# Kernel optimization log

Hardware: AMD Instinct MI355X
Metric: run time of the kernel (lower is better)

## Reference

```python
import jax, jax.numpy as jnp
import numpy as np

B, T_OBS, H, L, D = 4096, 8, 512, 2, 2


def _gates(x, h, c, Wih, Whh, b):
    # PyTorch LSTM gate order: i, f, g, o
    g = x @ Wih.T + h @ Whh.T + b
    i, f, gg, o = jnp.split(g, 4, axis=-1)
    c_new = jax.nn.sigmoid(f) * c + jax.nn.sigmoid(i) * jnp.tanh(gg)
    h_new = jax.nn.sigmoid(o) * jnp.tanh(c_new)
    return h_new, c_new


def _run_lstm(x, Wih, Whh, b):
    # stacked batch_first LSTM, zero initial state; x: [B,T,H]
    n_layers = Wih.shape[0]
    hs, cs = [], []
    for l in range(n_layers):
        def step(carry, xt, l=l):
            h, c = carry
            h, c = _gates(xt, h, c, Wih[l], Whh[l], b[l])
            return (h, c), h
        init = (jnp.zeros((x.shape[0], Whh.shape[-1]), x.dtype),
                jnp.zeros((x.shape[0], Whh.shape[-1]), x.dtype))
        (h, c), ys = jax.lax.scan(step, init, jnp.swapaxes(x, 0, 1))
        x = jnp.swapaxes(ys, 0, 1)
        hs.append(h)
        cs.append(c)
    return x, jnp.stack(hs), jnp.stack(cs)


def setup_inputs() -> dict:
    key = jax.random.key(0)
    ks = jax.random.split(key, 12)
    s = 1.0 / np.sqrt(H)
    inp = {
        "obs": jax.random.normal(ks[0], (B, T_OBS, D), jnp.float32),
        "obsVel": jax.random.normal(ks[1], (B, T_OBS, D), jnp.float32),
        "mean": jax.random.normal(ks[2], (D,), jnp.float32),
        "std": jnp.ones((D,), jnp.float32),
        "pred_len": 12,
        "enc_W": jax.random.normal(ks[3], (D, H), jnp.float32) * s,
        "enc_b": jnp.zeros((H,), jnp.float32),
        "dec_W": jax.random.normal(ks[4], (H, D), jnp.float32) * s,
        "dec_b": jnp.zeros((D,), jnp.float32),
        "lstm_Wih": jax.random.normal(ks[5], (L, 4 * H, H), jnp.float32) * s,
        "lstm_Whh": jax.random.normal(ks[6], (L, 4 * H, H), jnp.float32) * s,
        "lstm_b": jnp.zeros((L, 4 * H), jnp.float32),
        "cell_Wih": jax.random.normal(ks[7], (L, 4 * H, H), jnp.float32) * s,
        "cell_Whh": jax.random.normal(ks[8], (L, 4 * H, H), jnp.float32) * s,
        "cell_b": jnp.zeros((L, 4 * H), jnp.float32),
    }
    return inp


def reference(obs, obsVel, mean, std, pred_len, enc_W, enc_b, dec_W, dec_b,
              lstm_Wih, lstm_Whh, lstm_b, cell_Wih, cell_Whh, cell_b):
    inp = (obsVel - mean) / std                      # [B,T,2]
    embed = inp @ enc_W + enc_b                      # [B,T,H]
    output, hs, cs = _run_lstm(embed, lstm_Wih, lstm_Whh, lstm_b)
    inner = output[:, -1, :]                         # [B,H]

    def decode_step(carry, _):
        hs, cs, inner = carry
        def layer(inner, xs):
            Wih, Whh, b, h, c = xs
            h2, c2 = _gates(inner, h, c, Wih, Whh, b)
            return h2, (h2, c2)
        inner2, (hs2, cs2) = jax.lax.scan(
            layer, inner, (cell_Wih, cell_Whh, cell_b, hs, cs))
        return (hs2, cs2, inner2), inner2

    _, steps = jax.lax.scan(decode_step, (hs, cs, inner), None,
                            length=pred_len - 1)     # [P-1,B,H]
    predlist = jnp.concatenate([output[:, -1:, :], jnp.swapaxes(steps, 0, 1)],
                               axis=1)               # [B,P,H]
    outVelocity = predlist @ dec_W + dec_b           # [B,P,2]
    pred = outVelocity[:, :, :2] * std + mean
    pred = jnp.cumsum(pred, axis=1) + obs[:, -1:, :]
    return pred
```

## Files before the change

kernel.cpp:

```cpp
#include <hip/hip_runtime.h>
#include <hip/hip_bf16.h>

typedef __attribute__((ext_vector_type(8))) short bf16x8;
typedef __attribute__((ext_vector_type(4))) float f32x4;

#define MFMA16(a,b,c) __builtin_amdgcn_mfma_f32_16x16x32_bf16(a,b,c,0,0,0)

__device__ inline ushort f2bf(float f){
  union { float f; uint u; } v; v.f = f;
  uint r = v.u + 0x7FFFu + ((v.u >> 16) & 1u);
  return (ushort)(r >> 16);
}
__device__ inline float sigf(float x){ return 1.f/(1.f+__expf(-x)); }
__device__ inline float tanhf_(float x){ return 2.f/(1.f+__expf(-2.f*x)) - 1.f; }

__device__ inline void gload_lds16(const ushort* g, ushort* lds){
  __builtin_amdgcn_global_load_lds(
      (const __attribute__((address_space(1))) void*)g,
      (__attribute__((address_space(3))) void*)lds, 16, 0, 0);
}

__global__ void convert_weights(const float* __restrict__ s0, const float* __restrict__ s1,
                                const float* __restrict__ s2, const float* __restrict__ s3,
                                ushort* __restrict__ dst){
  size_t i4 = ((size_t)blockIdx.x*256 + threadIdx.x)*4;
  int tsel = (int)(i4 >> 21);
  const float* s = (tsel & 2) ? ((tsel & 1) ? s3 : s2) : ((tsel & 1) ? s1 : s0);
  size_t off = i4 & 2097151u;
  float4 v = *(const float4*)&s[off];
  ushort4 o; o.x=f2bf(v.x); o.y=f2bf(v.y); o.z=f2bf(v.z); o.w=f2bf(v.w);
  *(ushort4*)&dst[i4] = o;
}

__global__ void embed_kernel(const float* __restrict__ obsVel, const float* __restrict__ mean,
                             const float* __restrict__ stdv, const float* __restrict__ encW,
                             const float* __restrict__ encb, ushort* __restrict__ embed){
  int idx = blockIdx.x*256 + threadIdx.x;
  int row = idx >> 6, c8 = (idx & 63) * 8;
  float x0 = (obsVel[row*2+0] - mean[0]) / stdv[0];
  float x1 = (obsVel[row*2+1] - mean[1]) / stdv[1];
  ushort o[8];
  #pragma unroll
  for (int j=0;j<8;j++){
    int col = c8 + j;
    o[j] = f2bf(x0*encW[col] + x1*encW[512+col] + encb[col]);
  }
  *(uint4*)&embed[(size_t)row*512 + c8] = *(const uint4*)o;
}

#define NKT_SEG 8

__global__ __launch_bounds__(512, 2) void lstm_cell_kernel(
    const ushort* __restrict__ A0, int lda0,
    const ushort* __restrict__ A1, int lda1,
    const ushort* __restrict__ B0,
    const ushort* __restrict__ B1,
    const float*  __restrict__ bias,
    float* __restrict__ C,
    ushort* __restrict__ H0, int ldh0,
    ushort* __restrict__ H1, int ldh1,
    int nSeg, int czero)
{
  __shared__ ushort aL [3][8192];
  __shared__ ushort bLs[3][16384];
  const int tid = threadIdx.x;
  const int w = tid >> 6, lane = tid & 63;
  const int wr = w >> 2, wc = w & 3;
  const int bm = blockIdx.y * 128;
  const int bn = blockIdx.x * 64;

  const int r0 = bm + wr*64 + ((lane>>4)<<2);
  const int ccol = bn + wc*16 + (lane&15);
  float br[4], creg[4][4];
  #pragma unroll
  for (int g=0;g<4;g++) br[g] = bias[g*512 + ccol];
  if (czero){
    #pragma unroll
    for (int m=0;m<4;m++)
      #pragma unroll
      for (int reg=0;reg<4;reg++) creg[m][reg] = 0.f;
  } else {
    #pragma unroll
    for (int m=0;m<4;m++)
      #pragma unroll
      for (int reg=0;reg<4;reg++)
        creg[m][reg] = C[(size_t)(r0 + m*16 + reg)*512 + ccol];
  }

  f32x4 acc[4][4];
  #pragma unroll
  for (int m=0;m<4;m++)
    #pragma unroll
    for (int g=0;g<4;g++) acc[m][g] = (f32x4)0.f;

  int ar_[2], ac_[2], aO_[2];
  #pragma unroll
  for (int p=0;p<2;p++){
    int i = p*512 + tid;
    int r = i>>3, s = i&7;
    ar_[p] = r;  ac_[p] = s ^ (r&7);
    aO_[p] = (p*512 + (tid & ~63)) * 8;
  }
  int bfr_[4], bc_[4], bO_[4];
  #pragma unroll
  for (int p=0;p<4;p++){
    int i = p*512 + tid;
    int r = i>>3, s = i&7;
    bfr_[p] = ((r>>6)<<9) + bn + (r&63);
    bc_[p]  = s ^ (r&7);
    bO_[p]  = (p*512 + (tid & ~63)) * 8;
  }

  int aOff[4], bOff[4];
  #pragma unroll
  for (int m=0;m<4;m++){
    int ra = wr*64 + m*16 + (lane&15);
    aOff[m] = ra*64 + (((lane>>4)) ^ (ra&7))*8;
  }
  #pragma unroll
  for (int n=0;n<4;n++){
    int rb = n*64 + wc*16 + (lane&15);
    bOff[n] = rb*64 + (((lane>>4)) ^ (rb&7))*8;
  }

  #define STAGE_A(bi, kt) do { \
    const ushort* Aseg_ = ((kt) < NKT_SEG) ? A0 : A1; \
    const int lda_ = ((kt) < NKT_SEG) ? lda0 : lda1; \
    const int k0_ = ((kt) & 7) << 6; \
    gload_lds16(Aseg_ + (size_t)(bm + ar_[0])*lda_ + k0_ + ac_[0]*8, &aL[bi][aO_[0]]); \
    gload_lds16(Aseg_ + (size_t)(bm + ar_[1])*lda_ + k0_ + ac_[1]*8, &aL[bi][aO_[1]]); \
  } while(0)

  #define STAGE_B0(bi, kt) do { \
    const ushort* Bseg_ = ((kt) < NKT_SEG) ? B0 : B1; \
    const int k0_ = ((kt) & 7) << 6; \
    gload_lds16(Bseg_ + (size_t)bfr_[0]*512 + k0_ + bc_[0]*8, &bLs[bi][bO_[0]]); \
    gload_lds16(Bseg_ + (size_t)bfr_[1]*512 + k0_ + bc_[1]*8, &bLs[bi][bO_[1]]); \
  } while(0)

  #define STAGE_B1(bi, kt) do { \
    const ushort* Bseg_ = ((kt) < NKT_SEG) ? B0 : B1; \
    const int k0_ = ((kt) & 7) << 6; \
    gload_lds16(Bseg_ + (size_t)bfr_[2]*512 + k0_ + bc_[2]*8, &bLs[bi][bO_[2]]); \
    gload_lds16(Bseg_ + (size_t)bfr_[3]*512 + k0_ + bc_[3]*8, &bLs[bi][bO_[3]]); \
  } while(0)

  #define P1BODY(bic, bis, ktv, DOSTG) do { \
    _Pragma("unroll") \
    for (int m=0;m<4;m++){ \
      aF[m][0] = *(const bf16x8*)&aL[bic][aOff[m]]; \
      aF[m][1] = *(const bf16x8*)&aL[bic][aOff[m]^32]; \
    } \
    _Pragma("unroll") \
    for (int n=0;n<2;n++){ \
      bF[n][0] = *(const bf16x8*)&bLs[bic][bOff[n]]; \
      bF[n][1] = *(const bf16x8*)&bLs[bic][bOff[n]^32]; \
    } \
    if (DOSTG){ STAGE_A(bis, (ktv)+2); STAGE_B0(bis, (ktv)+2); } \
    asm volatile("s_waitcnt lgkmcnt(8)" ::: "memory"); \
    __builtin_amdgcn_s_barrier(); \
    asm volatile("s_waitcnt lgkmcnt(0)" ::: "memory"); \
    __builtin_amdgcn_sched_barrier(0); \
    __builtin_amdgcn_s_setprio(1); \
    _Pragma("unroll") \
    for (int kk=0;kk<2;kk++) \
      _Pragma("unroll") \
      for (int n=0;n<2;n++) \
        _Pragma("unroll") \
        for (int m=0;m<4;m++) \
          acc[m][n] = MFMA16(aF[m][kk], bF[n][kk], acc[m][n]); \
    __builtin_amdgcn_s_setprio(0); \
    __builtin_amdgcn_s_barrier(); \
  } while(0)

  #define P2BODY(bic, bis, ktv, DOSTG, VMN) do { \
    _Pragma("unroll") \
    for (int n=0;n<2;n++){ \
      bF[n][0] = *(const bf16x8*)&bLs[bic][bOff[n+2]]; \
      bF[n][1] = *(const bf16x8*)&bLs[bic][bOff[n+2]^32]; \
    } \
    if (DOSTG){ STAGE_B1(bis, (ktv)+2); } \
    asm volatile("s_waitcnt vmcnt(" #VMN ")" ::: "memory"); \
    __builtin_amdgcn_s_barrier(); \
    asm volatile("s_waitcnt lgkmcnt(0)" ::: "memory"); \
    __builtin_amdgcn_sched_barrier(0); \
    __builtin_amdgcn_s_setprio(1); \
    _Pragma("unroll") \
    for (int kk=0;kk<2;kk++) \
      _Pragma("unroll") \
      for (int n=0;n<2;n++) \
        _Pragma("unroll") \
        for (int m=0;m<4;m++) \
          acc[m][n+2] = MFMA16(aF[m][kk], bF[n][kk], acc[m][n+2]); \
    __builtin_amdgcn_s_setprio(0); \
    __builtin_amdgcn_s_barrier(); \
  } while(0)

  const int nkt = nSeg * NKT_SEG;
  int b0 = 0, b1 = 1, b2 = 2;
  bf16x8 aF[4][2], bF[2][2];

  STAGE_A(0, 0); STAGE_B0(0, 0); STAGE_B1(0, 0);
  STAGE_A(1, 1); STAGE_B0(1, 1); STAGE_B1(1, 1);
  asm volatile("s_waitcnt vmcnt(6)" ::: "memory");
  __builtin_amdgcn_s_barrier();

  for (int kt = 0; kt < nkt-2; ++kt){
    P1BODY(b0, b2, kt, 1);
    P2BODY(b0, b2, kt, 1, 6);
    int t_ = b0; b0 = b1; b1 = b2; b2 = t_;
  }
  P1BODY(b0, b2, 0, 0);
  P2BODY(b0, b2, 0, 0, 0);
  { int t_ = b0; b0 = b1; b1 = b2; b2 = t_; }
  P1BODY(b0, b2, 0, 0);
  P2BODY(b0, b2, 0, 0, 0);

  #undef STAGE_A
  #undef STAGE_B0
  #undef STAGE_B1
  #undef P1BODY
  #undef P2BODY

  #pragma unroll
  for (int m=0;m<4;m++){
    #pragma unroll
    for (int reg=0;reg<4;reg++){
      const int row = r0 + m*16 + reg;
      float gi = acc[m][0][reg] + br[0];
      float gf = acc[m][1][reg] + br[1];
      float gg = acc[m][2][reg] + br[2];
      float go = acc[m][3][reg] + br[3];
      float cn = sigf(gf)*creg[m][reg] + sigf(gi)*tanhf_(gg);
      float hv = sigf(go)*tanhf_(cn);
      C[(size_t)row*512 + ccol] = cn;
      ushort hb = f2bf(hv);
      H0[(size_t)row*ldh0 + ccol] = hb;
      if (H1) H1[(size_t)row*ldh1 + ccol] = hb;
    }
  }
}

__global__ void final_kernel(const ushort* __restrict__ pred, const float* __restrict__ decW,
                             const float* __restrict__ decb, const float* __restrict__ mean,
                             const float* __restrict__ stdv, const float* __restrict__ obs,
                             float* __restrict__ out){
  int w = threadIdx.x >> 6, lane = threadIdx.x & 63;
  int b = blockIdx.x*4 + w;
  float w0[8], w1[8];
  #pragma unroll
  for (int j=0;j<8;j++){
    int k = lane*8 + j;
    w0[j] = decW[k*2+0];
    w1[j] = decW[k*2+1];
  }
  float cum0 = 0.f, cum1 = 0.f;
  float m0 = mean[0], m1 = mean[1], sv0 = stdv[0], sv1 = stdv[1];
  float o0 = obs[(b*8+7)*2+0], o1 = obs[(b*8+7)*2+1];
  float db0 = decb[0], db1 = decb[1];
  for (int t=0;t<12;t++){
    const uint4 q = *(const uint4*)&pred[((size_t)b*12+t)*512 + lane*8];
    uint u[4] = {q.x,q.y,q.z,q.w};
    float s0=0.f, s1=0.f;
    #pragma unroll
    for (int p=0;p<4;p++){
      float lo = __uint_as_float(u[p]<<16);
      float hi = __uint_as_float(u[p]&0xffff0000u);
      s0 += lo*w0[2*p] + hi*w0[2*p+1];
      s1 += lo*w1[2*p] + hi*w1[2*p+1];
    }
    #pragma unroll
    for (int off=32; off>0; off>>=1){ s0 += __shfl_down(s0, off); s1 += __shfl_down(s1, off); }
    if (lane==0){
      cum0 += (s0+db0)*sv0 + m0;
      cum1 += (s1+db1)*sv1 + m1;
      out[((size_t)b*12+t)*2+0] = cum0 + o0;
      out[((size_t)b*12+t)*2+1] = cum1 + o1;
    }
  }
}

extern "C" void kernel_launch(void* const* d_in, const int* in_sizes, int n_in,
                              void* d_out, int out_size, void* d_ws, size_t ws_size,
                              hipStream_t stream) {
  const float* obs      = (const float*)d_in[0];
  const float* obsVel   = (const float*)d_in[1];
  const float* mean     = (const float*)d_in[2];
  const float* stdv     = (const float*)d_in[3];
  const float* encW     = (const float*)d_in[5];
  const float* encb     = (const float*)d_in[6];
  const float* decW     = (const float*)d_in[7];
  const float* decb     = (const float*)d_in[8];
  const float* lstm_Wih = (const float*)d_in[9];
  const float* lstm_Whh = (const float*)d_in[10];
  const float* lstm_b   = (const float*)d_in[11];
  const float* cell_Wih = (const float*)d_in[12];
  const float* cell_Whh = (const float*)d_in[13];
  const float* cell_b   = (const float*)d_in[14];

  char* ws = (char*)d_ws;
  ushort* wbf   = (ushort*)ws;
  ushort* embed = (ushort*)(ws + (16ull<<20));
  ushort* h0[2] = {(ushort*)(ws + (48ull<<20)), (ushort*)(ws + (52ull<<20))};
  ushort* h1[2] = {(ushort*)(ws + (56ull<<20)), (ushort*)(ws + (60ull<<20))};
  float*  c0    = (float*)(ws + (64ull<<20));
  float*  c1    = (float*)(ws + (72ull<<20));
  ushort* pred  = (ushort*)(ws + (80ull<<20));

  ushort* w_lstm_ih = wbf;
  ushort* w_lstm_hh = wbf + 2097152;
  ushort* w_cell_ih = wbf + 4194304;
  ushort* w_cell_hh = wbf + 6291456;

  convert_weights<<<8192, 256, 0, stream>>>(lstm_Wih, lstm_Whh, cell_Wih, cell_Whh, wbf);
  embed_kernel<<<8192, 256, 0, stream>>>(obsVel, mean, stdv, encW, encb, embed);

  dim3 grid(8, 32);
  int cur0 = 0, cur1 = 0;
  for (int t=0;t<8;t++){
    int ns = (t==0) ? 1 : 2;
    int cz = (t==0) ? 1 : 0;
    lstm_cell_kernel<<<grid, 512, 0, stream>>>(embed + t*512, 4096, h0[cur0], 512,
        w_lstm_ih, w_lstm_hh, lstm_b, c0, h0[cur0^1], 512, (ushort*)nullptr, 0, ns, cz);
    lstm_cell_kernel<<<grid, 512, 0, stream>>>(h0[cur0^1], 512, h1[cur1], 512,
        w_lstm_ih + 1048576, w_lstm_hh + 1048576, lstm_b + 2048, c1, h1[cur1^1], 512,
        (t==7) ? pred : (ushort*)nullptr, 6144, ns, cz);
    cur0 ^= 1; cur1 ^= 1;
  }
  for (int s=1;s<12;s++){
    lstm_cell_kernel<<<grid, 512, 0, stream>>>(pred + (s-1)*512, 6144, h0[cur0], 512,
        w_cell_ih, w_cell_hh, cell_b, c0, h0[cur0^1], 512, (ushort*)nullptr, 0, 2, 0);
    lstm_cell_kernel<<<grid, 512, 0, stream>>>(h0[cur0^1], 512, h1[cur1], 512,
        w_cell_ih + 1048576, w_cell_hh + 1048576, cell_b + 2048, c1, h1[cur1^1], 512,
        pred + s*512, 6144, 2, 0);
    cur0 ^= 1; cur1 ^= 1;
  }
  final_kernel<<<1024, 256, 0, stream>>>(pred, decW, decb, mean, stdv, obs, (float*)d_out);
}
```

Measured before the change: 982.1 us.

## Wavefront encoder layers into combined launches and fuse prep kernels

The encoder now runs layer-0 step t and layer-1 step t-1 in a single launch with a doubled grid, selecting per-block argument structs. This fills more compute units per launch and cuts the number of serial launches on the encoder path. The weight conversion and embedding kernels are merged into one prep launch. Passing the arguments as structs and selecting between them per block adds some register and scalar overhead.

```diff
diff --git a/kernel.cpp b/kernel.cpp
--- a/kernel.cpp
+++ b/kernel.cpp
@@ -20,61 +20,63 @@
       (__attribute__((address_space(3))) void*)lds, 16, 0, 0);
 }
 
-__global__ void convert_weights(const float* __restrict__ s0, const float* __restrict__ s1,
-                                const float* __restrict__ s2, const float* __restrict__ s3,
-                                ushort* __restrict__ dst){
-  size_t i4 = ((size_t)blockIdx.x*256 + threadIdx.x)*4;
-  int tsel = (int)(i4 >> 21);
-  const float* s = (tsel & 2) ? ((tsel & 1) ? s3 : s2) : ((tsel & 1) ? s1 : s0);
-  size_t off = i4 & 2097151u;
-  float4 v = *(const float4*)&s[off];
-  ushort4 o; o.x=f2bf(v.x); o.y=f2bf(v.y); o.z=f2bf(v.z); o.w=f2bf(v.w);
-  *(ushort4*)&dst[i4] = o;
-}
-
-__global__ void embed_kernel(const float* __restrict__ obsVel, const float* __restrict__ mean,
-                             const float* __restrict__ stdv, const float* __restrict__ encW,
-                             const float* __restrict__ encb, ushort* __restrict__ embed){
-  int idx = blockIdx.x*256 + threadIdx.x;
-  int row = idx >> 6, c8 = (idx & 63) * 8;
-  float x0 = (obsVel[row*2+0] - mean[0]) / stdv[0];
-  float x1 = (obsVel[row*2+1] - mean[1]) / stdv[1];
-  ushort o[8];
-  #pragma unroll
-  for (int j=0;j<8;j++){
-    int col = c8 + j;
-    o[j] = f2bf(x0*encW[col] + x1*encW[512+col] + encb[col]);
-  }
-  *(uint4*)&embed[(size_t)row*512 + c8] = *(const uint4*)o;
+__global__ void prep_kernel(const float* __restrict__ s0, const float* __restrict__ s1,
+                            const float* __restrict__ s2, const float* __restrict__ s3,
+                            ushort* __restrict__ dst,
+                            const float* __restrict__ obsVel, const float* __restrict__ mean,
+                            const float* __restrict__ stdv, const float* __restrict__ encW,
+                            const float* __restrict__ encb, ushort* __restrict__ embed){
+  if (blockIdx.x < 8192){
+    size_t i4 = ((size_t)blockIdx.x*256 + threadIdx.x)*4;
+    int tsel = (int)(i4 >> 21);
+    const float* s = (tsel & 2) ? ((tsel & 1) ? s3 : s2) : ((tsel & 1) ? s1 : s0);
+    size_t off = i4 & 2097151u;
+    float4 v = *(const float4*)&s[off];
+    ushort4 o; o.x=f2bf(v.x); o.y=f2bf(v.y); o.z=f2bf(v.z); o.w=f2bf(v.w);
+    *(ushort4*)&dst[i4] = o;
+  } else {
+    int idx = (blockIdx.x - 8192)*256 + threadIdx.x;
+    int row = idx >> 6, c8 = (idx & 63) * 8;
+    float x0 = (obsVel[row*2+0] - mean[0]) / stdv[0];
+    float x1 = (obsVel[row*2+1] - mean[1]) / stdv[1];
+    ushort o[8];
+    #pragma unroll
+    for (int j=0;j<8;j++){
+      int col = c8 + j;
+      o[j] = f2bf(x0*encW[col] + x1*encW[512+col] + encb[col]);
+    }
+    *(uint4*)&embed[(size_t)row*512 + c8] = *(const uint4*)o;
+  }
 }
 
 #define NKT_SEG 8
 
-__global__ __launch_bounds__(512, 2) void lstm_cell_kernel(
-    const ushort* __restrict__ A0, int lda0,
-    const ushort* __restrict__ A1, int lda1,
-    const ushort* __restrict__ B0,
-    const ushort* __restrict__ B1,
-    const float*  __restrict__ bias,
-    float* __restrict__ C,
-    ushort* __restrict__ H0, int ldh0,
-    ushort* __restrict__ H1, int ldh1,
-    int nSeg, int czero)
-{
+struct CellArgs {
+  const ushort *A0, *A1, *B0, *B1;
+  const float *bias;
+  float *C;
+  ushort *H0, *H1;
+  int lda0, lda1, ldh1, nSeg, czero;
+};
+
+__global__ __launch_bounds__(512, 2) void lstm_cell_kernel(CellArgs cA, CellArgs cB, int nyA){
   __shared__ ushort aL [3][8192];
   __shared__ ushort bLs[3][16384];
+  const bool isA = (int)blockIdx.y < nyA;
+  const CellArgs P = isA ? cA : cB;
+  const int by = isA ? blockIdx.y : (blockIdx.y - nyA);
   const int tid = threadIdx.x;
   const int w = tid >> 6, lane = tid & 63;
   const int wr = w >> 2, wc = w & 3;
-  const int bm = blockIdx.y * 128;
+  const int bm = by * 128;
   const int bn = blockIdx.x * 64;
 
   const int r0 = bm + wr*64 + ((lane>>4)<<2);
   const int ccol = bn + wc*16 + (lane&15);
   float br[4], creg[4][4];
   #pragma unroll
-  for (int g=0;g<4;g++) br[g] = bias[g*512 + ccol];
-  if (czero){
+  for (int g=0;g<4;g++) br[g] = P.bias[g*512 + ccol];
+  if (P.czero){
     #pragma unroll
     for (int m=0;m<4;m++)
       #pragma unroll
@@ -84,7 +86,7 @@
     for (int m=0;m<4;m++)
       #pragma unroll
       for (int reg=0;reg<4;reg++)
-        creg[m][reg] = C[(size_t)(r0 + m*16 + reg)*512 + ccol];
+        creg[m][reg] = P.C[(size_t)(r0 + m*16 + reg)*512 + ccol];
   }
 
   f32x4 acc[4][4];
@@ -124,22 +126,22 @@
   }
 
   #define STAGE_A(bi, kt) do { \
-    const ushort* Aseg_ = ((kt) < NKT_SEG) ? A0 : A1; \
-    const int lda_ = ((kt) < NKT_SEG) ? lda0 : lda1; \
+    const ushort* Aseg_ = ((kt) < NKT_SEG) ? P.A0 : P.A1; \
+    const int lda_ = ((kt) < NKT_SEG) ? P.lda0 : P.lda1; \
     const int k0_ = ((kt) & 7) << 6; \
     gload_lds16(Aseg_ + (size_t)(bm + ar_[0])*lda_ + k0_ + ac_[0]*8, &aL[bi][aO_[0]]); \
     gload_lds16(Aseg_ + (size_t)(bm + ar_[1])*lda_ + k0_ + ac_[1]*8, &aL[bi][aO_[1]]); \
   } while(0)
 
   #define STAGE_B0(bi, kt) do { \
-    const ushort* Bseg_ = ((kt) < NKT_SEG) ? B0 : B1; \
+    const ushort* Bseg_ = ((kt) < NKT_SEG) ? P.B0 : P.B1; \
     const int k0_ = ((kt) & 7) << 6; \
     gload_lds16(Bseg_ + (size_t)bfr_[0]*512 + k0_ + bc_[0]*8, &bLs[bi][bO_[0]]); \
     gload_lds16(Bseg_ + (size_t)bfr_[1]*512 + k0_ + bc_[1]*8, &bLs[bi][bO_[1]]); \
   } while(0)
 
   #define STAGE_B1(bi, kt) do { \
-    const ushort* Bseg_ = ((kt) < NKT_SEG) ? B0 : B1; \
+    const ushort* Bseg_ = ((kt) < NKT_SEG) ? P.B0 : P.B1; \
     const int k0_ = ((kt) & 7) << 6; \
     gload_lds16(Bseg_ + (size_t)bfr_[2]*512 + k0_ + bc_[2]*8, &bLs[bi][bO_[2]]); \
     gload_lds16(Bseg_ + (size_t)bfr_[3]*512 + k0_ + bc_[3]*8, &bLs[bi][bO_[3]]); \
@@ -196,7 +198,7 @@
     __builtin_amdgcn_s_barrier(); \
   } while(0)
 
-  const int nkt = nSeg * NKT_SEG;
+  const int nkt = P.nSeg * NKT_SEG;
   int b0 = 0, b1 = 1, b2 = 2;
   bf16x8 aF[4][2], bF[2][2];
 
@@ -233,10 +235,10 @@
       float go = acc[m][3][reg] + br[3];
       float cn = sigf(gf)*creg[m][reg] + sigf(gi)*tanhf_(gg);
       float hv = sigf(go)*tanhf_(cn);
-      C[(size_t)row*512 + ccol] = cn;
+      P.C[(size_t)row*512 + ccol] = cn;
       ushort hb = f2bf(hv);
-      H0[(size_t)row*ldh0 + ccol] = hb;
-      if (H1) H1[(size_t)row*ldh1 + ccol] = hb;
+      P.H0[(size_t)row*512 + ccol] = hb;
+      if (P.H1) P.H1[(size_t)row*P.ldh1 + ccol] = hb;
     }
   }
 }
@@ -301,39 +303,56 @@
   char* ws = (char*)d_ws;
   ushort* wbf   = (ushort*)ws;
   ushort* embed = (ushort*)(ws + (16ull<<20));
-  ushort* h0[2] = {(ushort*)(ws + (48ull<<20)), (ushort*)(ws + (52ull<<20))};
-  ushort* h1[2] = {(ushort*)(ws + (56ull<<20)), (ushort*)(ws + (60ull<<20))};
+  ushort* h0buf[2] = {(ushort*)(ws + (48ull<<20)), (ushort*)(ws + (52ull<<20))};
+  ushort* h1buf[2] = {(ushort*)(ws + (56ull<<20)), (ushort*)(ws + (60ull<<20))};
   float*  c0    = (float*)(ws + (64ull<<20));
   float*  c1    = (float*)(ws + (72ull<<20));
   ushort* pred  = (ushort*)(ws + (80ull<<20));
 
-  ushort* w_lstm_ih = wbf;
-  ushort* w_lstm_hh = wbf + 2097152;
-  ushort* w_cell_ih = wbf + 4194304;
-  ushort* w_cell_hh = wbf + 6291456;
-
-  convert_weights<<<8192, 256, 0, stream>>>(lstm_Wih, lstm_Whh, cell_Wih, cell_Whh, wbf);
-  embed_kernel<<<8192, 256, 0, stream>>>(obsVel, mean, stdv, encW, encb, embed);
-
-  dim3 grid(8, 32);
-  int cur0 = 0, cur1 = 0;
-  for (int t=0;t<8;t++){
-    int ns = (t==0) ? 1 : 2;
-    int cz = (t==0) ? 1 : 0;
-    lstm_cell_kernel<<<grid, 512, 0, stream>>>(embed + t*512, 4096, h0[cur0], 512,
-        w_lstm_ih, w_lstm_hh, lstm_b, c0, h0[cur0^1], 512, (ushort*)nullptr, 0, ns, cz);
-    lstm_cell_kernel<<<grid, 512, 0, stream>>>(h0[cur0^1], 512, h1[cur1], 512,
-        w_lstm_ih + 1048576, w_lstm_hh + 1048576, lstm_b + 2048, c1, h1[cur1^1], 512,
-        (t==7) ? pred : (ushort*)nullptr, 6144, ns, cz);
-    cur0 ^= 1; cur1 ^= 1;
-  }
-  for (int s=1;s<12;s++){
-    lstm_cell_kernel<<<grid, 512, 0, stream>>>(pred + (s-1)*512, 6144, h0[cur0], 512,
-        w_cell_ih, w_cell_hh, cell_b, c0, h0[cur0^1], 512, (ushort*)nullptr, 0, 2, 0);
-    lstm_cell_kernel<<<grid, 512, 0, stream>>>(h0[cur0^1], 512, h1[cur1], 512,
-        w_cell_ih + 1048576, w_cell_hh + 1048576, cell_b + 2048, c1, h1[cur1^1], 512,
-        pred + s*512, 6144, 2, 0);
-    cur0 ^= 1; cur1 ^= 1;
-  }
+  const ushort* wl_ih = wbf;
+  const ushort* wl_hh = wbf + 2097152;
+  const ushort* wc_ih = wbf + 4194304;
+  const ushort* wc_hh = wbf + 6291456;
+
+  prep_kernel<<<16384, 256, 0, stream>>>(lstm_Wih, lstm_Whh, cell_Wih, cell_Whh, wbf,
+                                         obsVel, mean, stdv, encW, encb, embed);
+
+  CellArgs L0[19], L1[19];
+  for (int t=0; t<19; ++t){
+    const bool enc = t < 8;
+    L0[t].A0   = enc ? embed + t*512 : pred + (t-8)*512;
+    L0[t].lda0 = enc ? 4096 : 6144;
+    L0[t].A1   = h0buf[t&1];  L0[t].lda1 = 512;
+    L0[t].B0   = enc ? wl_ih : wc_ih;
+    L0[t].B1   = enc ? wl_hh : wc_hh;
+    L0[t].bias = enc ? lstm_b : cell_b;
+    L0[t].C    = c0;
+    L0[t].H0   = h0buf[(t+1)&1];
+    L0[t].H1   = nullptr;  L0[t].ldh1 = 0;
+    L0[t].nSeg = (t==0) ? 1 : 2;
+    L0[t].czero= (t==0) ? 1 : 0;
+
+    L1[t].A0   = h0buf[(t+1)&1];  L1[t].lda0 = 512;
+    L1[t].A1   = h1buf[t&1];      L1[t].lda1 = 512;
+    L1[t].B0   = (enc ? wl_ih : wc_ih) + 1048576;
+    L1[t].B1   = (enc ? wl_hh : wc_hh) + 1048576;
+    L1[t].bias = (enc ? lstm_b : cell_b) + 2048;
+    L1[t].C    = c1;
+    L1[t].H0   = h1buf[(t+1)&1];
+    L1[t].H1   = enc ? (t==7 ? pred : nullptr) : pred + (t-7)*512;
+    L1[t].ldh1 = 6144;
+    L1[t].nSeg = (t==0) ? 1 : 2;
+    L1[t].czero= (t==0) ? 1 : 0;
+  }
+
+  lstm_cell_kernel<<<dim3(8,32), 512, 0, stream>>>(L0[0], L0[0], 32);
+  for (int t=1; t<8; ++t)
+    lstm_cell_kernel<<<dim3(8,64), 512, 0, stream>>>(L0[t], L1[t-1], 32);
+  lstm_cell_kernel<<<dim3(8,32), 512, 0, stream>>>(L1[7], L1[7], 32);
+  for (int t=8; t<19; ++t){
+    lstm_cell_kernel<<<dim3(8,32), 512, 0, stream>>>(L0[t], L0[t], 32);
+    lstm_cell_kernel<<<dim3(8,32), 512, 0, stream>>>(L1[t], L1[t], 32);
+  }
+
   final_kernel<<<1024, 256, 0, stream>>>(pred, decW, decb, mean, stdv, obs, (float*)d_out);
 }
```

Result: no change. 971.9 us (-1.0%).
